# Performance work log

Hardware: AMD Instinct MI355X
Metric: run time of the kernel (lower is better)

Reference implementation:

```python
import jax, jax.numpy as jnp
import numpy as np

IMG_W, IMG_H = 704, 256
BN_EPS, LN_EPS = 1e-5, 1e-5


def _l2norm(x, axis):
    n = jnp.linalg.norm(x, axis=axis, keepdims=True)
    return x / jnp.maximum(n, 1e-12)


def _layernorm(x, g, b):
    m = jnp.mean(x, axis=-1, keepdims=True)
    v = jnp.var(x, axis=-1, keepdims=True)
    return (x - m) / jnp.sqrt(v + LN_EPS) * g + b


def _bilinear(ref, uv):
    # ref: (B, d, H, W); uv: (B, P, 2) pixel coords (x, y)
    B, d, H, W = ref.shape
    x, y = uv[..., 0], uv[..., 1]
    x0 = jnp.floor(x); y0 = jnp.floor(y)
    wx = x - x0; wy = y - y0
    valid = (x >= 0) & (x <= W - 1) & (y >= 0) & (y <= H - 1)
    x0i = jnp.clip(x0.astype(jnp.int32), 0, W - 1)
    x1i = jnp.clip(x0i + 1, 0, W - 1)
    y0i = jnp.clip(y0.astype(jnp.int32), 0, H - 1)
    y1i = jnp.clip(y0i + 1, 0, H - 1)
    ref_t = ref.reshape(B, d, H * W).transpose(0, 2, 1)  # (B, HW, d)
    g = lambda yy, xx: jnp.take_along_axis(ref_t, (yy * W + xx)[..., None], axis=1)
    val = (g(y0i, x0i) * ((1 - wx) * (1 - wy))[..., None]
           + g(y0i, x1i) * (wx * (1 - wy))[..., None]
           + g(y1i, x0i) * ((1 - wx) * wy)[..., None]
           + g(y1i, x1i) * (wx * wy)[..., None])  # (B, P, d)
    return val, valid.astype(ref.dtype)


def setup_inputs() -> dict:
    key = jax.random.key(0)
    ks = jax.random.split(key, 12)
    b, n, fd, dim, h, w = 2, 6, 128, 128, 64, 176
    feature = jax.random.normal(ks[0], (b, n, fd, h, w), jnp.float32)
    # intrinsics ~ [[500,0,352],[0,500,128],[0,0,1]]
    K = jnp.array([[500.0, 0.0, IMG_W / 2], [0.0, 500.0, IMG_H / 2], [0.0, 0.0, 1.0]], jnp.float32)
    I_src = jnp.broadcast_to(K, (b, n, 3, 3)).copy()
    I_tar_inv = jnp.broadcast_to(jnp.linalg.inv(K), (b, 3, 3)).copy()
    # extrinsics near identity: small rotation + small translation
    a = 0.02 * jax.random.normal(ks[1], (b, n, 3), jnp.float32)
    zeros = jnp.zeros((b, n), jnp.float32)
    skew = jnp.stack([
        jnp.stack([zeros, -a[..., 2], a[..., 1]], -1),
        jnp.stack([a[..., 2], zeros, -a[..., 0]], -1),
        jnp.stack([-a[..., 1], a[..., 0], zeros], -1)], -2)
    R = jnp.eye(3, dtype=jnp.float32) + skew
    T = 0.1 * jax.random.normal(ks[2], (b, n, 3, 1), jnp.float32)
    E = jnp.broadcast_to(jnp.eye(4, dtype=jnp.float32), (b, n, 4, 4)).copy()
    E = E.at[..., :3, :3].set(R).at[..., :3, 3:4].set(T)
    dis = 1.5 * jnp.ones((b, 1, 1, 1), jnp.float32)
    norm = jnp.array([0.0, 0.0, 1.0], jnp.float32)[None, None] + 0.01 * jax.random.normal(ks[3], (b, 1, 3), jnp.float32)
    s = 1.0 / np.sqrt(fd)
    return {
        'feature': feature, 'I_src': I_src, 'I_tar_inv': I_tar_inv, 'E': E, 'dis': dis, 'norm': norm,
        'conv_w': s * jax.random.normal(ks[4], (dim, fd), jnp.float32),
        'bn_gamma': jnp.ones((fd,), jnp.float32), 'bn_beta': jnp.zeros((fd,), jnp.float32),
        'bn_mean': 0.1 * jax.random.normal(ks[5], (fd,), jnp.float32),
        'bn_var': jax.random.uniform(ks[6], (fd,), jnp.float32, 0.5, 1.5),
        'ln1_g': jnp.ones((dim,), jnp.float32), 'ln1_b': jnp.zeros((dim,), jnp.float32),
        'ln2_g': jnp.ones((dim,), jnp.float32), 'ln2_b': jnp.zeros((dim,), jnp.float32),
        'mlp_w1': s * jax.random.normal(ks[7], (dim, 2 * dim), jnp.float32),
        'mlp_b1': jnp.zeros((2 * dim,), jnp.float32),
        'mlp_w2': (1.0 / np.sqrt(2 * fd)) * jax.random.normal(ks[8], (2 * dim, dim), jnp.float32),
        'mlp_b2': jnp.zeros((dim,), jnp.float32),
    }


def reference(feature, I_src, I_tar_inv, E, dis, norm, conv_w, bn_gamma, bn_beta, bn_mean, bn_var,
              ln1_g, ln1_b, ln2_g, ln2_b, mlp_w1, mlp_b1, mlp_w2, mlp_b2):
    b, n, fd, h, w = feature.shape
    dim = conv_w.shape[0]
    P = h * w
    # ---- pixel grid in [0,1], homogeneous ----
    xs = jnp.linspace(0.0, 1.0, w, dtype=feature.dtype)
    ys = jnp.linspace(0.0, 1.0, h, dtype=feature.dtype)
    X, Y = jnp.meshgrid(xs, ys)  # (h, w), x varies along width
    pix = jnp.stack([X, Y, jnp.ones_like(X)], 0).reshape(3, P)  # (3, P)
    img_wh1 = jnp.array([[IMG_W], [IMG_H], [1.0]], feature.dtype)  # (3,1)
    pix = pix * img_wh1
    # ---- homography H = I_src (R - T n^T / dis) I_tar_inv ----
    R = E[..., :3, :3]
    T = E[..., :3, 3:4]
    Hm = I_src @ (R - (T @ norm[:, None, :, :]) / dis) @ I_tar_inv[:, None, :, :]  # (b,n,3,3)
    homo = jnp.einsum('bnij,jp->bnip', Hm, pix)  # (b,n,3,P)
    homo = homo[:, :, :2] / homo[:, :, 2:]
    homo = homo / img_wh1[:2]  # back to 0..1
    uv = homo.transpose(0, 1, 3, 2).reshape(b * n, P, 2) * jnp.array([w, h], feature.dtype)
    # ---- feature_linear: BN(eval) -> ReLU -> 1x1 conv ----
    xf = (feature - bn_mean[:, None, None]) / jnp.sqrt(bn_var + BN_EPS)[:, None, None]
    xf = xf * bn_gamma[:, None, None] + bn_beta[:, None, None]
    xf = jax.nn.relu(xf)
    val = jnp.einsum('oc,bnchw->bnohw', conv_w, xf)  # (b,n,dim,h,w)
    query = val[:, 0]  # (b,dim,h,w)
    # ---- homography-guided bilinear sampling ----
    v, mask = _bilinear(val.reshape(b * n, dim, h, w), uv)  # (bn,P,dim), (bn,P)
    key_n = _l2norm(v, axis=2).reshape(b, n, P, dim)
    q = _l2norm(query.reshape(b, dim, P), axis=1)
    dot = jnp.einsum('bdp,bnpd->bnp', q, key_n)
    dot = dot * mask.reshape(b, n, P)
    att = jax.nn.softmax(dot, axis=1)
    z = jnp.einsum('bnp,bnpd->bpd', att, v.reshape(b, n, P, dim))
    z = z.transpose(0, 2, 1).reshape(b, dim, h, w)
    z = query + z
    # ---- MLP block ----
    z = z.reshape(b, dim, P).transpose(0, 2, 1)  # (b,P,dim)
    z = _layernorm(z, ln1_g, ln1_b)
    hdn = jax.nn.gelu(z @ mlp_w1 + mlp_b1, approximate=False)
    z = z + (hdn @ mlp_w2 + mlp_b2)
    z = _layernorm(z, ln2_g, ln2_b)
    return z.transpose(0, 2, 1).reshape(b, dim, h, w)
```

## Files before the change

### kernel.cpp

```cpp
#include <hip/hip_runtime.h>
#include <hip/hip_bf16.h>
#include <cstdint>
#include <cstddef>

#define B_   2
#define N_   6
#define FD_  128
#define DIM_ 128
#define H_   64
#define W_   176
#define P_   (H_*W_)
#define IMGW 704.0
#define IMGH 256.0

struct __align__(16) Samp { float wx, wy; int o00, o01; int o10, o11; int valid, pad; };

typedef __attribute__((ext_vector_type(8))) short short8;
typedef __attribute__((ext_vector_type(4))) float f32x4;

__device__ __forceinline__ float wave_sum(float v) {
#pragma unroll
  for (int off = 32; off > 0; off >>= 1) v += __shfl_xor(v, off, 64);
  return v;
}

__device__ __forceinline__ unsigned short f2bf(float f) {
  union { __hip_bfloat16 h; unsigned short u; } c;
  c.h = __float2bfloat16(f);
  return c.u;
}
__device__ __forceinline__ float bf2f(unsigned short s) {
  return __uint_as_float(((unsigned int)s) << 16);
}

__global__ __launch_bounds__(256) void prep_kernel(const float* __restrict__ I_src, const float* __restrict__ I_tar_inv,
                           const float* __restrict__ E, const float* __restrict__ dis,
                           const float* __restrict__ nrm,
                           const float* __restrict__ bn_g, const float* __restrict__ bn_b,
                           const float* __restrict__ bn_m, const float* __restrict__ bn_v,
                           const float* __restrict__ w1, const float* __restrict__ w2,
                           const float* __restrict__ conv_w,
                           Samp* __restrict__ samp, float* __restrict__ bns, float* __restrict__ bnb,
                           short* __restrict__ w1b, short* __restrict__ w2b, short* __restrict__ cwb) {
  int blk = blockIdx.x;
  if (blk >= B_ * N_) {
    int tid = (blk - B_ * N_) * 256 + threadIdx.x;
    int f = tid >> 6, l = tid & 63;
    if (f < 64) {
      int nt = f >> 2, ks = f & 3;
      int n = nt * 16 + (l & 15);
      int kb = ks * 32 + (l >> 4) * 8;
#pragma unroll
      for (int j = 0; j < 8; ++j)
        w1b[((size_t)f * 64 + l) * 8 + j] = (short)f2bf(w1[(size_t)(kb + j) * 256 + n]);
    } else if (f < 128) {
      int g = f - 64;
      int nt = g >> 3, ks = g & 7;
      int n = nt * 16 + (l & 15);
      int kb = ks * 32 + (l >> 4) * 8;
#pragma unroll
      for (int j = 0; j < 8; ++j)
        w2b[((size_t)g * 64 + l) * 8 + j] = (short)f2bf(w2[(size_t)(kb + j) * 128 + n]);
    } else {
      int g2 = f - 128;
      int ot = g2 >> 2, ks = g2 & 3;
      int o  = ot * 16 + (l & 15);
      int cb = ks * 32 + (l >> 4) * 8;
#pragma unroll
      for (int j = 0; j < 8; ++j)
        cwb[((size_t)g2 * 64 + l) * 8 + j] = (short)f2bf(conv_w[(size_t)o * FD_ + cb + j]);
    }
    return;
  }
  int bn = blk;
  int bb = bn / N_;
  if (bn == 0 && threadIdx.x < FD_) {
    int t = threadIdx.x;
    float inv = 1.0f / sqrtf(bn_v[t] + 1e-5f);
    float sc = bn_g[t] * inv;
    bns[t] = sc;
    bnb[t] = bn_b[t] - bn_m[t] * sc;
  }
  const float* Ep = E + bn * 16;
  double R[9], T[3];
#pragma unroll
  for (int i = 0; i < 3; ++i) {
#pragma unroll
    for (int j = 0; j < 3; ++j) R[i*3+j] = (double)Ep[i*4+j];
    T[i] = (double)Ep[i*4+3];
  }
  double dd = (double)dis[bb];
  double M[9];
#pragma unroll
  for (int i = 0; i < 3; ++i)
#pragma unroll
    for (int j = 0; j < 3; ++j)
      M[i*3+j] = R[i*3+j] - T[i] * (double)nrm[bb*3+j] / dd;
  const float* Is = I_src + bn * 9;
  double A[9];
#pragma unroll
  for (int i = 0; i < 3; ++i)
#pragma unroll
    for (int j = 0; j < 3; ++j)
      A[i*3+j] = (double)Is[i*3+0]*M[0+j] + (double)Is[i*3+1]*M[3+j] + (double)Is[i*3+2]*M[6+j];
  const float* It = I_tar_inv + bb * 9;
  double Hm[9];
#pragma unroll
  for (int i = 0; i < 3; ++i)
#pragma unroll
    for (int j = 0; j < 3; ++j)
      Hm[i*3+j] = A[i*3+0]*(double)It[0+j] + A[i*3+1]*(double)It[3+j] + A[i*3+2]*(double)It[6+j];

  const double dx = 1.0 / (double)(W_ - 1);
  const double dy = 1.0 / (double)(H_ - 1);
  for (int p = threadIdx.x; p < P_; p += 256) {
    int ii = p / W_;
    int jj = p - ii * W_;
    double xs = (jj == W_ - 1) ? 1.0 : (double)jj * dx;
    double ys = (ii == H_ - 1) ? 1.0 : (double)ii * dy;
    double px = xs * IMGW;
    double py = ys * IMGH;
    double hx = Hm[0]*px + Hm[1]*py + Hm[2];
    double hy = Hm[3]*px + Hm[4]*py + Hm[5];
    double hz = Hm[6]*px + Hm[7]*py + Hm[8];
    double u = ((hx / hz) / IMGW) * (double)W_;
    double v = ((hy / hz) / IMGH) * (double)H_;
    double x0 = floor(u), y0 = floor(v);
    bool valid = (u >= 0.0) && (u <= (double)(W_ - 1)) && (v >= 0.0) && (v <= (double)(H_ - 1));
    int x0i = min(max((int)x0, 0), W_ - 1);
    int x1i = min(x0i + 1, W_ - 1);
    int y0i = min(max((int)y0, 0), H_ - 1);
    int y1i = min(y0i + 1, H_ - 1);
    Samp s;
    s.wx = (float)(u - x0);
    s.wy = (float)(v - y0);
    s.o00 = (y0i * W_ + x0i) * DIM_;
    s.o01 = (y0i * W_ + x1i) * DIM_;
    s.o10 = (y1i * W_ + x0i) * DIM_;
    s.o11 = (y1i * W_ + x1i) * DIM_;
    s.valid = valid ? 1 : 0;
    s.pad = 0;
    samp[(size_t)bn * P_ + p] = s;
  }
}

__global__ __launch_bounds__(256) void conv_kernel(const float* __restrict__ feature,
    const short* __restrict__ cwb, const float* __restrict__ bns_g, const float* __restrict__ bnb_g,
    unsigned short* __restrict__ val_t) {
  __shared__ __align__(16) short xhi[128 * 66];
  __shared__ __align__(16) short xlo[128 * 66];
  __shared__ float bns_s[FD_], bnb_s[FD_];
  int t = threadIdx.x;

  if (t < FD_) { bns_s[t] = bns_g[t]; bnb_s[t] = bnb_g[t]; }
  __syncthreads();

  int bn = blockIdx.y;
  int p0 = blockIdx.x * 64;
  const float* fb = feature + (size_t)bn * FD_ * P_ + p0;

#pragma unroll
  for (int k = 0; k < 8; ++k) {
    int f4 = t + 256 * k;
    int c  = f4 >> 4;
    int pq = (f4 & 15) * 4;
    float4 x = *(const float4*)(fb + (size_t)c * P_ + pq);
    float s = bns_s[c], o = bnb_s[c];
    float v0 = fmaxf(x.x * s + o, 0.f);
    float v1 = fmaxf(x.y * s + o, 0.f);
    float v2 = fmaxf(x.z * s + o, 0.f);
    float v3 = fmaxf(x.w * s + o, 0.f);
    unsigned short h0 = f2bf(v0), h1 = f2bf(v1), h2 = f2bf(v2), h3 = f2bf(v3);
    unsigned short l0 = f2bf(v0 - bf2f(h0)), l1 = f2bf(v1 - bf2f(h1));
    unsigned short l2 = f2bf(v2 - bf2f(h2)), l3 = f2bf(v3 - bf2f(h3));
    short* dh = &xhi[c * 66 + pq];
    short* dl = &xlo[c * 66 + pq];
    dh[0] = (short)h0; dh[1] = (short)h1; dh[2] = (short)h2; dh[3] = (short)h3;
    dl[0] = (short)l0; dl[1] = (short)l1; dl[2] = (short)l2; dl[3] = (short)l3;
  }
  __syncthreads();

  int lane = t & 63, wv = t >> 6;
  int m = lane & 15, quad = lane >> 4;
  int pw = wv * 16;

  short8 Ah[4], Al[4];
#pragma unroll
  for (int ks = 0; ks < 4; ++ks) {
#pragma unroll
    for (int j = 0; j < 8; ++j) {
      int c = ks * 32 + quad * 8 + j;
      Ah[ks][j] = xhi[c * 66 + pw + m];
      Al[ks][j] = xlo[c * 66 + pw + m];
    }
  }

  f32x4 acc[8];
#pragma unroll
  for (int ot = 0; ot < 8; ++ot) {
    f32x4 a = {0.f, 0.f, 0.f, 0.f};
#pragma unroll
    for (int ks = 0; ks < 4; ++ks) {
      short8 Bv = *(const short8*)(cwb + ((size_t)(ot * 4 + ks) * 64 + lane) * 8);
      a = __builtin_amdgcn_mfma_f32_16x16x32_bf16(Ah[ks], Bv, a, 0, 0, 0);
      a = __builtin_amdgcn_mfma_f32_16x16x32_bf16(Al[ks], Bv, a, 0, 0, 0);
    }
    acc[ot] = a;
  }

  unsigned short* vb = val_t + ((size_t)bn * P_ + p0 + pw + quad * 4) * DIM_ + m;
#pragma unroll
  for (int ot = 0; ot < 8; ++ot)
#pragma unroll
    for (int r = 0; r < 4; ++r)
      vb[(size_t)r * DIM_ + ot * 16] = f2bf(acc[ot][r]);
}

__global__ __launch_bounds__(256) void attn_kernel(const unsigned short* __restrict__ val_t,
    const Samp* __restrict__ samp,
    const float* __restrict__ ln1g, const float* __restrict__ ln1b,
    float* __restrict__ zln) {
  int lane = threadIdx.x & 63;
  int wv = threadIdx.x >> 6;
  int bid = blockIdx.x;
  int newbid = (bid & 7) * (gridDim.x >> 3) + (bid >> 3);
  int pt = newbid * 4 + wv;
  if (pt >= B_ * P_) return;
  int bb = pt / P_;
  int p = pt - bb * P_;
  int d0 = lane << 1;

  unsigned int uq = *(const unsigned int*)(val_t + ((size_t)(bb * N_) * P_ + p) * DIM_ + d0);
  float qx = bf2f((unsigned short)(uq & 0xffffu));
  float qy = bf2f((unsigned short)(uq >> 16));
  float qss = wave_sum(qx * qx + qy * qy);
  float qinv = 1.0f / fmaxf(sqrtf(qss), 1e-12f);
  float qn0 = qx * qinv, qn1 = qy * qinv;

  float dots[N_], vs0[N_], vs1[N_];
#pragma unroll
  for (int n = 0; n < N_; ++n) {
    Samp s = samp[(size_t)(bb * N_ + n) * P_ + p];
    const unsigned short* base = val_t + (size_t)(bb * N_ + n) * P_ * DIM_ + d0;
    unsigned int u00 = *(const unsigned int*)(base + s.o00);
    unsigned int u01 = *(const unsigned int*)(base + s.o01);
    unsigned int u10 = *(const unsigned int*)(base + s.o10);
    unsigned int u11 = *(const unsigned int*)(base + s.o11);
    float wx = s.wx, wy = s.wy;
    float w00 = (1.0f - wx) * (1.0f - wy), w01 = wx * (1.0f - wy);
    float w10 = (1.0f - wx) * wy,          w11 = wx * wy;
    float v0 = bf2f((unsigned short)(u00 & 0xffffu)) * w00 + bf2f((unsigned short)(u01 & 0xffffu)) * w01
             + bf2f((unsigned short)(u10 & 0xffffu)) * w10 + bf2f((unsigned short)(u11 & 0xffffu)) * w11;
    float v1 = bf2f((unsigned short)(u00 >> 16)) * w00 + bf2f((unsigned short)(u01 >> 16)) * w01
             + bf2f((unsigned short)(u10 >> 16)) * w10 + bf2f((unsigned short)(u11 >> 16)) * w11;
    float ss = wave_sum(v0 * v0 + v1 * v1);
    float kinv = 1.0f / fmaxf(sqrtf(ss), 1e-12f);
    float dt = wave_sum(qn0 * (v0 * kinv) + qn1 * (v1 * kinv));
    dots[n] = s.valid ? dt : 0.0f;
    vs0[n] = v0; vs1[n] = v1;
  }
  float mx = dots[0];
#pragma unroll
  for (int n = 1; n < N_; ++n) mx = fmaxf(mx, dots[n]);
  float es[N_], den = 0.f;
#pragma unroll
  for (int n = 0; n < N_; ++n) { es[n] = expf(dots[n] - mx); den += es[n]; }
  float dinv = 1.0f / den;
  float z0 = qx, z1 = qy;
#pragma unroll
  for (int n = 0; n < N_; ++n) { float a = es[n] * dinv; z0 += a * vs0[n]; z1 += a * vs1[n]; }
  float mean = wave_sum(z0 + z1) * (1.0f / DIM_);
  float c0 = z0 - mean, c1 = z1 - mean;
  float var = wave_sum(c0 * c0 + c1 * c1) * (1.0f / DIM_);
  float rstd = rsqrtf(var + 1e-5f);
  float o0 = c0 * rstd * ln1g[d0]     + ln1b[d0];
  float o1 = c1 * rstd * ln1g[d0 + 1] + ln1b[d0 + 1];
  *(float2*)(zln + (size_t)pt * DIM_ + d0) = make_float2(o0, o1);
}

__global__ __launch_bounds__(512) void mlp_kernel(const float* __restrict__ zln,
    const short* __restrict__ w1b, const short* __restrict__ w2b,
    const float* __restrict__ b1, const float* __restrict__ b2,
    const float* __restrict__ ln2g, const float* __restrict__ ln2b,
    float* __restrict__ out) {
  __shared__ __align__(16) char smem[34816];
  int t = threadIdx.x;
  int row0 = blockIdx.x * 64;

  float* zl = (float*)smem;
#pragma unroll
  for (int k = 0; k < 4; ++k) {
    int idx = t + 512 * k;
    int r = idx >> 5, c4 = (idx & 31) * 4;
    *(float4*)&zl[r * 132 + c4] = *(const float4*)(zln + (size_t)(row0 + r) * DIM_ + c4);
  }
  __syncthreads();

  int lane = t & 63, wv = t >> 6, m = lane & 15, quad = lane >> 4;
  int pt = wv & 3, ng = wv >> 2;
  int pw = pt * 16;

  short8 A1h[4], A1l[4];
#pragma unroll
  for (int ks = 0; ks < 4; ++ks) {
    const float* zr = &zl[(pw + m) * 132 + ks * 32 + quad * 8];
#pragma unroll
    for (int j = 0; j < 8; ++j) {
      float v = zr[j];
      unsigned short h = f2bf(v);
      A1h[ks][j] = (short)h;
      A1l[ks][j] = (short)f2bf(v - bf2f(h));
    }
  }
  float res[4][4];
#pragma unroll
  for (int i = 0; i < 4; ++i)
#pragma unroll
    for (int r = 0; r < 4; ++r)
      res[i][r] = zl[(pw + quad * 4 + r) * 132 + (ng * 4 + i) * 16 + m];

  float b1v[2][4];
#pragma unroll
  for (int h = 0; h < 2; ++h)
#pragma unroll
    for (int i = 0; i < 4; ++i) b1v[h][i] = b1[(h * 8 + ng * 4 + i) * 16 + m];
  float b2v[4], g2v[4], be2v[4];
#pragma unroll
  for (int i = 0; i < 4; ++i) {
    int d = (ng * 4 + i) * 16 + m;
    b2v[i] = b2[d]; g2v[i] = ln2g[d]; be2v[i] = ln2b[d];
  }
  __syncthreads();

  short* hh = (short*)smem;
  short* hl = (short*)(smem + 17408);

  f32x4 acc2[4];
#pragma unroll
  for (int i = 0; i < 4; ++i) acc2[i] = (f32x4){0.f, 0.f, 0.f, 0.f};

#pragma unroll
  for (int h = 0; h < 2; ++h) {
    if (h) __syncthreads();
#pragma unroll
    for (int i = 0; i < 4; ++i) {
      int nt = h * 8 + ng * 4 + i;
      f32x4 a = {0.f, 0.f, 0.f, 0.f};
#pragma unroll
      for (int ks = 0; ks < 4; ++ks) {
        short8 Bv = *(const short8*)(w1b + ((size_t)(nt * 4 + ks) * 64 + lane) * 8);
        a = __builtin_amdgcn_mfma_f32_16x16x32_bf16(A1h[ks], Bv, a, 0, 0, 0);
        a = __builtin_amdgcn_mfma_f32_16x16x32_bf16(A1l[ks], Bv, a, 0, 0, 0);
      }
#pragma unroll
      for (int r = 0; r < 4; ++r) {
        float hv = a[r] + b1v[h][i];
        float g = 0.5f * hv * (1.0f + erff(hv * 0.70710678118654752f));
        unsigned short gh = f2bf(g);
        int addr = (pw + quad * 4 + r) * 136 + (ng * 4 + i) * 16 + m;
        hh[addr] = (short)gh;
        hl[addr] = (short)f2bf(g - bf2f(gh));
      }
    }
    __syncthreads();
#pragma unroll
    for (int ks2 = 0; ks2 < 4; ++ks2) {
      short8 A2h = *(const short8*)&hh[(pw + m) * 136 + ks2 * 32 + quad * 8];
      short8 A2l = *(const short8*)&hl[(pw + m) * 136 + ks2 * 32 + quad * 8];
#pragma unroll
      for (int i = 0; i < 4; ++i) {
        int g = (ng * 4 + i) * 8 + h * 4 + ks2;
        short8 Bv = *(const short8*)(w2b + ((size_t)g * 64 + lane) * 8);
        acc2[i] = __builtin_amdgcn_mfma_f32_16x16x32_bf16(A2h, Bv, acc2[i], 0, 0, 0);
        acc2[i] = __builtin_amdgcn_mfma_f32_16x16x32_bf16(A2l, Bv, acc2[i], 0, 0, 0);
      }
    }
  }

  float z2[4][4];
#pragma unroll
  for (int i = 0; i < 4; ++i)
#pragma unroll
    for (int r = 0; r < 4; ++r)
      z2[i][r] = acc2[i][r] + b2v[i] + res[i][r];

  __syncthreads();
  float* pbuf = (float*)smem;
  float ps[4];
#pragma unroll
  for (int r = 0; r < 4; ++r) {
    float s = z2[0][r] + z2[1][r] + z2[2][r] + z2[3][r];
    s += __shfl_xor(s, 1, 64); s += __shfl_xor(s, 2, 64);
    s += __shfl_xor(s, 4, 64); s += __shfl_xor(s, 8, 64);
    ps[r] = s;
  }
  if (m == 0) {
#pragma unroll
    for (int r = 0; r < 4; ++r) pbuf[ng * 64 + pw + quad * 4 + r] = ps[r];
  }
  __syncthreads();
  float mean[4];
#pragma unroll
  for (int r = 0; r < 4; ++r) {
    int px = pw + quad * 4 + r;
    mean[r] = (pbuf[px] + pbuf[64 + px]) * (1.0f / 128.0f);
  }
  float pv[4];
#pragma unroll
  for (int r = 0; r < 4; ++r) {
    float vv = 0.f;
#pragma unroll
    for (int i = 0; i < 4; ++i) { float d = z2[i][r] - mean[r]; vv += d * d; }
    vv += __shfl_xor(vv, 1, 64); vv += __shfl_xor(vv, 2, 64);
    vv += __shfl_xor(vv, 4, 64); vv += __shfl_xor(vv, 8, 64);
    pv[r] = vv;
  }
  if (m == 0) {
#pragma unroll
    for (int r = 0; r < 4; ++r) pbuf[128 + ng * 64 + pw + quad * 4 + r] = pv[r];
  }
  __syncthreads();
  float rstd[4];
#pragma unroll
  for (int r = 0; r < 4; ++r) {
    int px = pw + quad * 4 + r;
    rstd[r] = rsqrtf((pbuf[128 + px] + pbuf[192 + px]) * (1.0f / 128.0f) + 1e-5f);
  }

  __syncthreads();
  float* zo = (float*)smem;
#pragma unroll
  for (int i = 0; i < 4; ++i)
#pragma unroll
    for (int r = 0; r < 4; ++r) {
      float v = (z2[i][r] - mean[r]) * rstd[r] * g2v[i] + be2v[i];
      zo[((ng * 4 + i) * 16 + m) * 68 + pw + quad * 4 + r] = v;
    }
  __syncthreads();

  int bb2 = row0 / P_;
  int p0 = row0 - bb2 * P_;
#pragma unroll
  for (int it = 0; it < 4; ++it) {
    int d = it * 32 + (t >> 4);
    int pq = (t & 15) * 4;
    float4 v4 = *(float4*)&zo[d * 68 + pq];
    *(float4*)(out + (size_t)bb2 * DIM_ * P_ + (size_t)d * P_ + p0 + pq) = v4;
  }
}

extern "C" void kernel_launch(void* const* d_in, const int* in_sizes, int n_in,
                              void* d_out, int out_size, void* d_ws, size_t ws_size,
                              hipStream_t stream) {
  const float* feature = (const float*)d_in[0];
  const float* I_src   = (const float*)d_in[1];
  const float* I_tar   = (const float*)d_in[2];
  const float* E       = (const float*)d_in[3];
  const float* dis     = (const float*)d_in[4];
  const float* nrm     = (const float*)d_in[5];
  const float* conv_w  = (const float*)d_in[6];
  const float* bn_g    = (const float*)d_in[7];
  const float* bn_b    = (const float*)d_in[8];
  const float* bn_m    = (const float*)d_in[9];
  const float* bn_v    = (const float*)d_in[10];
  const float* ln1g    = (const float*)d_in[11];
  const float* ln1b    = (const float*)d_in[12];
  const float* ln2g    = (const float*)d_in[13];
  const float* ln2b    = (const float*)d_in[14];
  const float* w1      = (const float*)d_in[15];
  const float* b1      = (const float*)d_in[16];
  const float* w2      = (const float*)d_in[17];
  const float* b2      = (const float*)d_in[18];
  float* out = (float*)d_out;

  float* wsf = (float*)d_ws;
  float* bns = wsf;
  float* bnb = wsf + 128;
  unsigned short* val_t = (unsigned short*)(wsf + 256);
  float* zln = (float*)(val_t + (size_t)B_ * N_ * P_ * DIM_);
  Samp*  samp = (Samp*)(zln + (size_t)B_ * P_ * DIM_);
  short* w1b = (short*)(samp + (size_t)B_ * N_ * P_);
  short* w2b = w1b + 32768;
  short* cwb = w2b + 32768;

  hipLaunchKernelGGL(prep_kernel, dim3(B_ * N_ + 40), dim3(256), 0, stream,
                     I_src, I_tar, E, dis, nrm, bn_g, bn_b, bn_m, bn_v, w1, w2, conv_w,
                     samp, bns, bnb, w1b, w2b, cwb);
  hipLaunchKernelGGL(conv_kernel, dim3(P_ / 64, B_ * N_), dim3(256), 0, stream,
                     feature, cwb, bns, bnb, val_t);
  hipLaunchKernelGGL(attn_kernel, dim3(B_ * P_ / 4), dim3(256), 0, stream,
                     val_t, samp, ln1g, ln1b, zln);
  hipLaunchKernelGGL(mlp_kernel, dim3(B_ * P_ / 64), dim3(512), 0, stream,
                     zln, w1b, w2b, b1, b2, ln2g, ln2b, out);
}
```

Baseline: 214.3 us.

## Split homography prep across blocks, vectorize conv stores, fuse attention reductions

The homography/sample-table prep now uses four blocks per camera instead of one, so the double-precision per-pixel work is spread over more CUs. The conv MFMA operands are swapped so each lane holds four consecutive output channels for one pixel, which lets the bf16 results go out as one 8-byte store instead of four scattered 2-byte stores. In attention, the key-norm and raw-dot reductions are merged into one shuffle loop, and normalization is applied afterwards as scalar multiplies. This halves the wave reductions per camera. It slightly changes rounding order.

Result: slower. 225.8 us (+5.4%).

```diff
diff --git a/kernel.cpp b/kernel.cpp
--- a/kernel.cpp
+++ b/kernel.cpp
@@ -12,6 +12,7 @@
 #define P_   (H_*W_)
 #define IMGW 704.0
 #define IMGH 256.0
+#define UVB  4
 
 struct __align__(16) Samp { float wx, wy; int o00, o01; int o10, o11; int valid, pad; };
 
@@ -43,8 +44,8 @@
                            Samp* __restrict__ samp, float* __restrict__ bns, float* __restrict__ bnb,
                            short* __restrict__ w1b, short* __restrict__ w2b, short* __restrict__ cwb) {
   int blk = blockIdx.x;
-  if (blk >= B_ * N_) {
-    int tid = (blk - B_ * N_) * 256 + threadIdx.x;
+  if (blk >= B_ * N_ * UVB) {
+    int tid = (blk - B_ * N_ * UVB) * 256 + threadIdx.x;
     int f = tid >> 6, l = tid & 63;
     if (f < 64) {
       int nt = f >> 2, ks = f & 3;
@@ -72,9 +73,10 @@
     }
     return;
   }
-  int bn = blk;
+  int bn = blk >> 2;
+  int part = blk & (UVB - 1);
   int bb = bn / N_;
-  if (bn == 0 && threadIdx.x < FD_) {
+  if (blk == 0 && threadIdx.x < FD_) {
     int t = threadIdx.x;
     float inv = 1.0f / sqrtf(bn_v[t] + 1e-5f);
     float sc = bn_g[t] * inv;
@@ -113,7 +115,7 @@
 
   const double dx = 1.0 / (double)(W_ - 1);
   const double dy = 1.0 / (double)(H_ - 1);
-  for (int p = threadIdx.x; p < P_; p += 256) {
+  for (int p = part * 256 + threadIdx.x; p < P_; p += 256 * UVB) {
     int ii = p / W_;
     int jj = p - ii * W_;
     double xs = (jj == W_ - 1) ? 1.0 : (double)jj * dx;
@@ -184,14 +186,14 @@
   int m = lane & 15, quad = lane >> 4;
   int pw = wv * 16;
 
-  short8 Ah[4], Al[4];
+  short8 Xh[4], Xl[4];
 #pragma unroll
   for (int ks = 0; ks < 4; ++ks) {
 #pragma unroll
     for (int j = 0; j < 8; ++j) {
       int c = ks * 32 + quad * 8 + j;
-      Ah[ks][j] = xhi[c * 66 + pw + m];
-      Al[ks][j] = xlo[c * 66 + pw + m];
+      Xh[ks][j] = xhi[c * 66 + pw + m];
+      Xl[ks][j] = xlo[c * 66 + pw + m];
     }
   }
 
@@ -201,19 +203,21 @@
     f32x4 a = {0.f, 0.f, 0.f, 0.f};
 #pragma unroll
     for (int ks = 0; ks < 4; ++ks) {
-      short8 Bv = *(const short8*)(cwb + ((size_t)(ot * 4 + ks) * 64 + lane) * 8);
-      a = __builtin_amdgcn_mfma_f32_16x16x32_bf16(Ah[ks], Bv, a, 0, 0, 0);
-      a = __builtin_amdgcn_mfma_f32_16x16x32_bf16(Al[ks], Bv, a, 0, 0, 0);
+      short8 Wv = *(const short8*)(cwb + ((size_t)(ot * 4 + ks) * 64 + lane) * 8);
+      a = __builtin_amdgcn_mfma_f32_16x16x32_bf16(Wv, Xh[ks], a, 0, 0, 0);
+      a = __builtin_amdgcn_mfma_f32_16x16x32_bf16(Wv, Xl[ks], a, 0, 0, 0);
     }
     acc[ot] = a;
   }
 
-  unsigned short* vb = val_t + ((size_t)bn * P_ + p0 + pw + quad * 4) * DIM_ + m;
-#pragma unroll
-  for (int ot = 0; ot < 8; ++ot)
-#pragma unroll
-    for (int r = 0; r < 4; ++r)
-      vb[(size_t)r * DIM_ + ot * 16] = f2bf(acc[ot][r]);
+  unsigned short* vb = val_t + ((size_t)bn * P_ + p0 + pw + m) * DIM_ + quad * 4;
+#pragma unroll
+  for (int ot = 0; ot < 8; ++ot) {
+    f32x4 a = acc[ot];
+    unsigned int lo = (unsigned int)f2bf(a[0]) | ((unsigned int)f2bf(a[1]) << 16);
+    unsigned int hi = (unsigned int)f2bf(a[2]) | ((unsigned int)f2bf(a[3]) << 16);
+    *(uint2*)(vb + ot * 16) = make_uint2(lo, hi);
+  }
 }
 
 __global__ __launch_bounds__(256) void attn_kernel(const unsigned short* __restrict__ val_t,
@@ -235,7 +239,6 @@
   float qy = bf2f((unsigned short)(uq >> 16));
   float qss = wave_sum(qx * qx + qy * qy);
   float qinv = 1.0f / fmaxf(sqrtf(qss), 1e-12f);
-  float qn0 = qx * qinv, qn1 = qy * qinv;
 
   float dots[N_], vs0[N_], vs1[N_];
 #pragma unroll
@@ -253,10 +256,15 @@
              + bf2f((unsigned short)(u10 & 0xffffu)) * w10 + bf2f((unsigned short)(u11 & 0xffffu)) * w11;
     float v1 = bf2f((unsigned short)(u00 >> 16)) * w00 + bf2f((unsigned short)(u01 >> 16)) * w01
              + bf2f((unsigned short)(u10 >> 16)) * w10 + bf2f((unsigned short)(u11 >> 16)) * w11;
-    float ss = wave_sum(v0 * v0 + v1 * v1);
+    float ss = v0 * v0 + v1 * v1;
+    float du = qx * v0 + qy * v1;
+#pragma unroll
+    for (int off = 32; off > 0; off >>= 1) {
+      ss += __shfl_xor(ss, off, 64);
+      du += __shfl_xor(du, off, 64);
+    }
     float kinv = 1.0f / fmaxf(sqrtf(ss), 1e-12f);
-    float dt = wave_sum(qn0 * (v0 * kinv) + qn1 * (v1 * kinv));
-    dots[n] = s.valid ? dt : 0.0f;
+    dots[n] = s.valid ? (du * kinv * qinv) : 0.0f;
     vs0[n] = v0; vs1[n] = v1;
   }
   float mx = dots[0];
@@ -483,7 +491,7 @@
   short* w2b = w1b + 32768;
   short* cwb = w2b + 32768;
 
-  hipLaunchKernelGGL(prep_kernel, dim3(B_ * N_ + 40), dim3(256), 0, stream,
+  hipLaunchKernelGGL(prep_kernel, dim3(B_ * N_ * UVB + 40), dim3(256), 0, stream,
                      I_src, I_tar, E, dis, nrm, bn_g, bn_b, bn_m, bn_v, w1, w2, conv_w,
                      samp, bns, bnb, w1b, w2b, cwb);
   hipLaunchKernelGGL(conv_kernel, dim3(P_ / 64, B_ * N_), dim3(256), 0, stream,
```
